# Performance work log

Hardware: AMD Instinct MI355X
Metric: run time of the kernel (lower is better)

The kernel has to match this reference:

```python
import jax, jax.numpy as jnp
import numpy as np

N, H, L, O = 8192, 512, 3, 512
LN_EPS = 1e-5


def setup_inputs() -> dict:
    key = jax.random.key(0)
    ks = jax.random.split(key, 8)
    # sparse symmetric adjacency with positive weights, zero diagonal
    u = jax.random.uniform(ks[0], (N, N))
    w = jax.random.uniform(ks[1], (N, N)) * 0.9 + 0.1
    A = jnp.where(u < 0.004, w, 0.0)
    A = (A + A.T) * 0.5
    A = A * (1.0 - jnp.eye(N, dtype=A.dtype))
    s = 0.02
    return {
        "node_feat": jax.random.normal(ks[2], (1, N, H), jnp.float32),
        "adj": A[None],
        "conv_w": jax.random.normal(ks[3], (L, H, H), jnp.float32) * s,
        "conv_b": jnp.zeros((L, H), jnp.float32),
        "mlp_w": jax.random.normal(ks[4], (L, H, H), jnp.float32) * s,
        "mlp_b": jnp.zeros((L, H), jnp.float32),
        "ln_g": jnp.ones((L, H), jnp.float32),
        "ln_b": jnp.zeros((L, H), jnp.float32),
        "lin_w": jax.random.normal(ks[5], (H, O), jnp.float32) * s,
        "lin_b": jnp.zeros((O,), jnp.float32),
    }


def _layer_norm(x, g, b):
    mu = jnp.mean(x, axis=-1, keepdims=True)
    var = jnp.mean(jnp.square(x - mu), axis=-1, keepdims=True)
    return (x - mu) * jax.lax.rsqrt(var + LN_EPS) * g + b


def reference(node_feat, adj, conv_w, conv_b, mlp_w, mlp_b, ln_g, ln_b, lin_w, lin_b):
    x = node_feat[0]          # [N, H]
    A = adj[0]                # [N, N]
    A = jnp.where(A > 0, A, 0.0)  # edges are positive entries only
    # gcn_norm: add self-loops (weight 1) only where missing
    d = jnp.diagonal(A)
    A1 = A + jnp.diag(jnp.where(d > 0, 0.0, 1.0))
    # deg scattered at target (edge_index[1] = column)
    deg = jnp.sum(A1, axis=0)
    dinv = jnp.where(deg > 0, deg ** -0.5, 0.0)
    Ahat = dinv[:, None] * A1 * dinv[None, :]  # [N, N]
    for l in range(L):
        # GCNConv: linear, propagate (aggregate at col), bias
        x = Ahat.T @ (x @ conv_w[l]) + conv_b[l]
        # MLP: Linear -> LayerNorm -> ReLU
        x = jax.nn.relu(_layer_norm(x @ mlp_w[l] + mlp_b[l], ln_g[l], ln_b[l]))
    mu = (x @ lin_w + lin_b)[None]  # [1, N, O]
    return mu
```

## Files before the change

### kernel.cpp

```cpp
#include <hip/hip_runtime.h>

#define NN 8192
#define HD 512
#define NL 3
#define CAP 128
#define NWB (273 * NL)
#define LN_EPS 1e-5f

typedef _Float16 f16;
typedef _Float16 f16x8 __attribute__((ext_vector_type(8)));
typedef _Float16 f16x4 __attribute__((ext_vector_type(4)));
typedef _Float16 f16x2 __attribute__((ext_vector_type(2)));
typedef float f32x4 __attribute__((ext_vector_type(4)));

__device__ __forceinline__ unsigned short f16_bits(f16 h) {
  union { f16 h; unsigned short u; } x; x.h = h; return x.u;
}
__device__ __forceinline__ f16 bits_f16(unsigned short u) {
  union { unsigned short u; f16 h; } x; x.u = u; return x.h;
}

__global__ __launch_bounds__(256) void k_prep(const float* __restrict__ A,
                                              const float* __restrict__ x0,
                                              const float* __restrict__ convw,
                                              const float* __restrict__ mlpw,
                                              const float* __restrict__ convb,
                                              const float* __restrict__ mlpb,
                                              const float* __restrict__ lw,
                                              unsigned* __restrict__ ell,
                                              int* __restrict__ nnz8,
                                              float* __restrict__ dinv,
                                              f16* __restrict__ xs,
                                              f16* __restrict__ WlT,
                                              float* __restrict__ bl,
                                              f16* __restrict__ lwT) {
  const int b = blockIdx.x;
  const int t = threadIdx.x;

  if (b < NWB) {
    const int l = b / 273;
    const int bx = b % 273;
    if (bx < 256) {
      const int m0 = bx * 2;
      const float* Wc = convw + (size_t)l * HD * HD;
      const float* Wm = mlpw + (size_t)l * HD * HD;
      f16* o = WlT + (size_t)l * HD * HD;
      float a00 = 0.f, a01 = 0.f, a10 = 0.f, a11 = 0.f;
      const float* wc0 = Wc + (size_t)m0 * HD;
      const float* wc1 = Wc + (size_t)(m0 + 1) * HD;
      for (int k = 0; k < HD; k++) {
        const float w0 = Wm[(size_t)k * HD + t];
        const float w1 = Wm[(size_t)k * HD + t + 256];
        const float c0 = wc0[k];
        const float c1 = wc1[k];
        a00 = fmaf(c0, w0, a00);
        a01 = fmaf(c0, w1, a01);
        a10 = fmaf(c1, w0, a10);
        a11 = fmaf(c1, w1, a11);
      }
      o[(size_t)t * HD + m0] = (f16)a00;
      o[(size_t)(t + 256) * HD + m0] = (f16)a01;
      o[(size_t)t * HD + m0 + 1] = (f16)a10;
      o[(size_t)(t + 256) * HD + m0 + 1] = (f16)a11;
    } else if (bx == 256) {
      const float* Wm = mlpw + (size_t)l * HD * HD;
      float acc0 = mlpb[l * HD + t];
      float acc1 = mlpb[l * HD + t + 256];
      for (int k = 0; k < HD; k++) {
        const float cb = convb[l * HD + k];
        acc0 = fmaf(cb, Wm[(size_t)k * HD + t], acc0);
        acc1 = fmaf(cb, Wm[(size_t)k * HD + t + 256], acc1);
      }
      bl[l * HD + t] = acc0;
      bl[l * HD + t + 256] = acc1;
    } else if (l == 0) {
      const int base = (bx - 257) * 16384;
      #pragma unroll 4
      for (int j = 0; j < 64; j++) {
        const int idx = base + j * 256 + t;
        const int k = idx >> 9, n = idx & 511;
        lwT[(size_t)n * HD + k] = (f16)lw[idx];
      }
    }
    return;
  }

  __shared__ int wtot[4];
  __shared__ float wsum[4];
  __shared__ float sdinv;
  const int r = b - NWB;
  const int lane = t & 63;
  const int wv = t >> 6;
  const float4* ar = (const float4*)(A + (size_t)r * NN);
  unsigned* er = ell + (size_t)r * CAP;
  const int rot = (r * 5) & 2047;

  int c = 0;
  float s = 0.f;
  #pragma unroll
  for (int i = 0; i < 8; i++) {
    const int f = (t + i * 256 + rot) & 2047;
    const float4 v = ar[f];
    c += (v.x > 0.f) + (v.y > 0.f) + (v.z > 0.f) + (v.w > 0.f);
    s += v.x + v.y + v.z + v.w;
  }
  int inc = c;
  #pragma unroll
  for (int d = 1; d < 64; d <<= 1) {
    int vv = __shfl_up(inc, d);
    if (lane >= d) inc += vv;
  }
  float ss = s;
  #pragma unroll
  for (int m = 1; m < 64; m <<= 1) ss += __shfl_xor(ss, m);
  if (lane == 63) wtot[wv] = inc;
  if (lane == 0) wsum[wv] = ss;
  __syncthreads();
  int base = inc - c;
  for (int w = 0; w < wv; w++) base += wtot[w];

  int o = base;
  #pragma unroll
  for (int i = 0; i < 8; i++) {
    const int f = (t + i * 256 + rot) & 2047;
    const float4 v = ar[f];
    float vals[4] = {v.x, v.y, v.z, v.w};
    #pragma unroll
    for (int q = 0; q < 4; q++) {
      float val = vals[q];
      if (val > 0.f) {
        if (o < CAP) er[o] = ((unsigned)f16_bits((f16)val) << 16) | (unsigned)(f * 4 + q);
        o++;
      }
    }
  }
  if (t == 255) {
    int ne = wtot[0] + wtot[1] + wtot[2] + wtot[3];
    if (ne < CAP) er[ne] = (0x3C00u << 16) | (unsigned)r;
    int ne1 = ne + 1; if (ne1 > CAP) ne1 = CAP;
    int n8 = (ne1 + 7) & ~7;
    for (int k = ne1; k < n8; k++) er[k] = (unsigned)r;
    nnz8[r] = n8;
    float deg = wsum[0] + wsum[1] + wsum[2] + wsum[3] + 1.f;
    float di = rsqrtf(deg);
    dinv[r] = di;
    sdinv = di;
  }
  __syncthreads();
  {
    const float di = sdinv;
    const float2 xv = ((const float2*)(x0 + (size_t)r * HD))[t];
    f16x2 o2 = {(f16)(xv.x * di), (f16)(xv.y * di)};
    ((f16x2*)(xs + (size_t)r * HD))[t] = o2;
  }
}

__global__ __launch_bounds__(256) void k_spmm(const unsigned* __restrict__ ell,
                                              const int* __restrict__ nnz8,
                                              const float* __restrict__ dinv,
                                              const f16* __restrict__ xs,
                                              f16* __restrict__ y) {
  const int bid = blockIdx.x;
  const int chunk = bid & 3;
  const int rb = bid >> 2;
  const int r = __builtin_amdgcn_readfirstlane(rb * 4 + (threadIdx.x >> 6));
  const int lane = threadIdx.x & 63;
  const int c0 = chunk * 128 + lane * 2;
  const uint4* er = (const uint4*)(ell + (size_t)r * CAP);
  const int ne = nnz8[r];
  const f16* xc = xs + c0;
  float a0 = 0.f, a1 = 0.f;
  for (int e8 = 0; e8 < (ne >> 3); e8++) {
    const uint4 ea = er[e8 * 2];
    const uint4 eb = er[e8 * 2 + 1];
    unsigned wv[8] = {ea.x, ea.y, ea.z, ea.w, eb.x, eb.y, eb.z, eb.w};
    f16x2 xv[8];
    #pragma unroll
    for (int q = 0; q < 8; q++)
      xv[q] = *(const f16x2*)(xc + (size_t)(wv[q] & 0xFFFFu) * HD);
    #pragma unroll
    for (int q = 0; q < 8; q++) {
      const float fw = (float)bits_f16((unsigned short)(wv[q] >> 16));
      a0 = fmaf(fw, (float)xv[q][0], a0);
      a1 = fmaf(fw, (float)xv[q][1], a1);
    }
  }
  const float s = dinv[r];
  f16x2 o = {(f16)(a0 * s), (f16)(a1 * s)};
  *(f16x2*)(y + (size_t)r * HD + c0) = o;
}

__global__ __launch_bounds__(512) void k_gemm_ln(const f16* __restrict__ y,
                                                 const f16* __restrict__ WT,
                                                 const float* __restrict__ bias,
                                                 const float* __restrict__ g,
                                                 const float* __restrict__ bb,
                                                 const float* __restrict__ dscale,
                                                 f16* __restrict__ outp) {
  __shared__ float red[32][4][2];
  const int t = threadIdx.x;
  const int lane = t & 63;
  const int w = t >> 6;
  const int wm = w >> 2;
  const int wn = w & 3;
  const int m0 = blockIdx.x * 32;
  const int rl = lane & 15, kg = (lane >> 4) * 8;
  const f16* aP = y + (size_t)(m0 + wm * 16 + rl) * HD + kg;
  const f16* bP = WT + (size_t)(wn * 128 + rl) * HD + kg;

  f32x4 acc[8];
  #pragma unroll
  for (int j = 0; j < 8; j++) { f32x4 z = {0.f, 0.f, 0.f, 0.f}; acc[j] = z; }

  #pragma unroll 2
  for (int ks = 0; ks < HD; ks += 32) {
    const f16x8 af = *(const f16x8*)(aP + ks);
    #pragma unroll
    for (int j = 0; j < 8; j++) {
      const f16x8 bf = *(const f16x8*)(bP + (size_t)j * 16 * HD + ks);
      acc[j] = __builtin_amdgcn_mfma_f32_16x16x32_f16(af, bf, acc[j], 0, 0, 0);
    }
  }

  const int cg = lane >> 4, cl = lane & 15;
  float av[8][4];
  #pragma unroll
  for (int j = 0; j < 8; j++) {
    const float bv = bias[wn * 128 + j * 16 + cl];
    #pragma unroll
    for (int r = 0; r < 4; r++) av[j][r] = acc[j][r] + bv;
  }
  #pragma unroll
  for (int r = 0; r < 4; r++) {
    float s = 0.f, sq = 0.f;
    #pragma unroll
    for (int j = 0; j < 8; j++) { s += av[j][r]; sq += av[j][r] * av[j][r]; }
    #pragma unroll
    for (int m = 1; m < 16; m <<= 1) { s += __shfl_xor(s, m); sq += __shfl_xor(sq, m); }
    if (cl == 0) {
      red[wm * 16 + cg * 4 + r][wn][0] = s;
      red[wm * 16 + cg * 4 + r][wn][1] = sq;
    }
  }
  __syncthreads();
  #pragma unroll
  for (int r = 0; r < 4; r++) {
    const int rb = wm * 16 + cg * 4 + r;
    float s = 0.f, sq = 0.f;
    #pragma unroll
    for (int q = 0; q < 4; q++) { s += red[rb][q][0]; sq += red[rb][q][1]; }
    const float mu = s * (1.f / HD);
    const float rs = rsqrtf(sq * (1.f / HD) - mu * mu + LN_EPS);
    const int row = m0 + rb;
    const float dsc = dscale ? dscale[row] : 1.f;
    #pragma unroll
    for (int j = 0; j < 8; j++) {
      const int col = wn * 128 + j * 16 + cl;
      const float val = fmaxf((av[j][r] - mu) * rs * g[col] + bb[col], 0.f) * dsc;
      outp[(size_t)row * HD + col] = (f16)val;
    }
  }
}

__global__ __launch_bounds__(256) void k_gemm_direct(const f16* __restrict__ A,
                                                     const f16* __restrict__ BT,
                                                     float* __restrict__ C,
                                                     const float* __restrict__ bias) {
  const int t = threadIdx.x;
  const int lane = t & 63;
  const int wave = t >> 6;
  const int wm = wave >> 1, wn = wave & 1;
  const int m0 = blockIdx.x * 128, n0 = blockIdx.y * 128;
  const int rl = lane & 15, kg = (lane >> 4) * 8;

  const f16* aP[4];
  const f16* bP[4];
  #pragma unroll
  for (int i = 0; i < 4; i++)
    aP[i] = A + (size_t)(m0 + wm * 64 + i * 16 + rl) * HD + kg;
  #pragma unroll
  for (int j = 0; j < 4; j++)
    bP[j] = BT + (size_t)(n0 + wn * 64 + j * 16 + rl) * HD + kg;

  f32x4 acc[4][4];
  #pragma unroll
  for (int i = 0; i < 4; i++)
    #pragma unroll
    for (int j = 0; j < 4; j++) {
      f32x4 z = {0.f, 0.f, 0.f, 0.f};
      acc[i][j] = z;
    }

  #pragma unroll 4
  for (int ks = 0; ks < HD; ks += 32) {
    f16x8 af[4], bf[4];
    #pragma unroll
    for (int i = 0; i < 4; i++) af[i] = *(const f16x8*)(aP[i] + ks);
    #pragma unroll
    for (int j = 0; j < 4; j++) bf[j] = *(const f16x8*)(bP[j] + ks);
    #pragma unroll
    for (int i = 0; i < 4; i++)
      #pragma unroll
      for (int j = 0; j < 4; j++)
        acc[i][j] = __builtin_amdgcn_mfma_f32_16x16x32_f16(af[i], bf[j], acc[i][j], 0, 0, 0);
  }

  const int cg = lane >> 4, cl = lane & 15;
  #pragma unroll
  for (int i = 0; i < 4; i++) {
    #pragma unroll
    for (int j = 0; j < 4; j++) {
      const int col = n0 + wn * 64 + j * 16 + cl;
      const float bv = bias ? bias[col] : 0.f;
      #pragma unroll
      for (int rr = 0; rr < 4; rr++) {
        const int row = m0 + wm * 64 + i * 16 + cg * 4 + rr;
        C[(size_t)row * HD + col] = acc[i][j][rr] + bv;
      }
    }
  }
}

extern "C" void kernel_launch(void* const* d_in, const int* in_sizes, int n_in,
                              void* d_out, int out_size, void* d_ws, size_t ws_size,
                              hipStream_t stream) {
  const float* node_feat = (const float*)d_in[0];
  const float* adj       = (const float*)d_in[1];
  const float* conv_w    = (const float*)d_in[2];
  const float* conv_b    = (const float*)d_in[3];
  const float* mlp_w     = (const float*)d_in[4];
  const float* mlp_b     = (const float*)d_in[5];
  const float* ln_g      = (const float*)d_in[6];
  const float* ln_b      = (const float*)d_in[7];
  const float* lin_w     = (const float*)d_in[8];
  const float* lin_b     = (const float*)d_in[9];
  float* out = (float*)d_out;

  char* p = (char*)d_ws;
  unsigned* ell = (unsigned*)p; p += (size_t)NN * CAP * 4;
  int* nnz8  = (int*)p;   p += (size_t)NN * 4;
  float* dinv = (float*)p; p += (size_t)NN * 4;
  f16* xsA   = (f16*)p;   p += (size_t)NN * HD * 2;
  f16* xsB   = (f16*)p;   p += (size_t)NN * HD * 2;
  f16* ybuf  = (f16*)p;   p += (size_t)NN * HD * 2;
  f16* WlT   = (f16*)p;   p += (size_t)NL * HD * HD * 2;
  f16* lwT   = (f16*)p;   p += (size_t)HD * HD * 2;
  float* bl  = (float*)p; p += (size_t)NL * HD * 4;

  k_prep<<<NWB + NN, 256, 0, stream>>>(adj, node_feat, conv_w, mlp_w,
                                       conv_b, mlp_b, lin_w,
                                       ell, nnz8, dinv, xsA, WlT, bl, lwT);

  f16* xcur = xsA;
  for (int l = 0; l < NL; l++) {
    k_spmm<<<NN, 256, 0, stream>>>(ell, nnz8, dinv, xcur, ybuf);
    f16* nxt = (xcur == xsA) ? xsB : xsA;
    k_gemm_ln<<<NN / 32, 512, 0, stream>>>(ybuf, WlT + (size_t)l * HD * HD,
                                           bl + l * HD, ln_g + l * HD, ln_b + l * HD,
                                           (l < 2) ? dinv : nullptr, nxt);
    xcur = nxt;
  }
  k_gemm_direct<<<dim3(64, 4), 256, 0, stream>>>(xcur, lwT, out, lin_b);
}
```

Baseline: 332.5 us.

## Split adjacency row scan into four segment blocks with separate degree kernel

The prep kernel now scans each adjacency row with four blocks, one per 2048-column segment, instead of one block per row. Each segment writes its own ELL slice of capacity 48 and stores a partial degree sum. A new small kernel combines the partial sums into dinv and scales the input features. The aim is more memory-level parallelism on the dominant 256 MB adjacency read. In exchange it adds a kernel launch, per-segment padding that the SpMM must loop over, and a per-segment overflow cap that could drop edges in a dense segment.

```diff
diff --git a/kernel.cpp b/kernel.cpp
--- a/kernel.cpp
+++ b/kernel.cpp
@@ -3,7 +3,8 @@
 #define NN 8192
 #define HD 512
 #define NL 3
-#define CAP 128
+#define CAPQ 48
+#define CAPR (4 * CAPQ)
 #define NWB (273 * NL)
 #define LN_EPS 1e-5f
 
@@ -21,16 +22,14 @@
 }
 
 __global__ __launch_bounds__(256) void k_prep(const float* __restrict__ A,
-                                              const float* __restrict__ x0,
                                               const float* __restrict__ convw,
                                               const float* __restrict__ mlpw,
                                               const float* __restrict__ convb,
                                               const float* __restrict__ mlpb,
                                               const float* __restrict__ lw,
                                               unsigned* __restrict__ ell,
-                                              int* __restrict__ nnz8,
-                                              float* __restrict__ dinv,
-                                              f16* __restrict__ xs,
+                                              int* __restrict__ nnz8q,
+                                              float* __restrict__ psum,
                                               f16* __restrict__ WlT,
                                               float* __restrict__ bl,
                                               f16* __restrict__ lwT) {
@@ -87,23 +86,20 @@
 
   __shared__ int wtot[4];
   __shared__ float wsum[4];
-  __shared__ float sdinv;
-  const int r = b - NWB;
+  const int sb = b - NWB;
+  const int r = sb >> 2;
+  const int seg = sb & 3;
   const int lane = t & 63;
   const int wv = t >> 6;
-  const float4* ar = (const float4*)(A + (size_t)r * NN);
-  unsigned* er = ell + (size_t)r * CAP;
-  const int rot = (r * 5) & 2047;
-
-  int c = 0;
-  float s = 0.f;
-  #pragma unroll
-  for (int i = 0; i < 8; i++) {
-    const int f = (t + i * 256 + rot) & 2047;
-    const float4 v = ar[f];
-    c += (v.x > 0.f) + (v.y > 0.f) + (v.z > 0.f) + (v.w > 0.f);
-    s += v.x + v.y + v.z + v.w;
-  }
+  const float4* aseg = (const float4*)(A + (size_t)r * NN + seg * 2048);
+  unsigned* er = ell + (size_t)r * CAPR + seg * CAPQ;
+
+  const float4 v0 = aseg[t];
+  const float4 v1 = aseg[t + 256];
+  int c = (v0.x > 0.f) + (v0.y > 0.f) + (v0.z > 0.f) + (v0.w > 0.f) +
+          (v1.x > 0.f) + (v1.y > 0.f) + (v1.z > 0.f) + (v1.w > 0.f);
+  float s = v0.x + v0.y + v0.z + v0.w + v1.x + v1.y + v1.z + v1.w;
+
   int inc = c;
   #pragma unroll
   for (int d = 1; d < 64; d <<= 1) {
@@ -120,43 +116,59 @@
   for (int w = 0; w < wv; w++) base += wtot[w];
 
   int o = base;
-  #pragma unroll
-  for (int i = 0; i < 8; i++) {
-    const int f = (t + i * 256 + rot) & 2047;
-    const float4 v = ar[f];
-    float vals[4] = {v.x, v.y, v.z, v.w};
+  const int cb0 = seg * 2048 + t * 4;
+  const int cb1 = seg * 2048 + (t + 256) * 4;
+  {
+    float vals[4] = {v0.x, v0.y, v0.z, v0.w};
     #pragma unroll
     for (int q = 0; q < 4; q++) {
-      float val = vals[q];
-      if (val > 0.f) {
-        if (o < CAP) er[o] = ((unsigned)f16_bits((f16)val) << 16) | (unsigned)(f * 4 + q);
+      if (vals[q] > 0.f) {
+        if (o < CAPQ) er[o] = ((unsigned)f16_bits((f16)vals[q]) << 16) | (unsigned)(cb0 + q);
+        o++;
+      }
+    }
+  }
+  {
+    float vals[4] = {v1.x, v1.y, v1.z, v1.w};
+    #pragma unroll
+    for (int q = 0; q < 4; q++) {
+      if (vals[q] > 0.f) {
+        if (o < CAPQ) er[o] = ((unsigned)f16_bits((f16)vals[q]) << 16) | (unsigned)(cb1 + q);
         o++;
       }
     }
   }
   if (t == 255) {
     int ne = wtot[0] + wtot[1] + wtot[2] + wtot[3];
-    if (ne < CAP) er[ne] = (0x3C00u << 16) | (unsigned)r;
-    int ne1 = ne + 1; if (ne1 > CAP) ne1 = CAP;
-    int n8 = (ne1 + 7) & ~7;
-    for (int k = ne1; k < n8; k++) er[k] = (unsigned)r;
-    nnz8[r] = n8;
-    float deg = wsum[0] + wsum[1] + wsum[2] + wsum[3] + 1.f;
-    float di = rsqrtf(deg);
-    dinv[r] = di;
-    sdinv = di;
-  }
-  __syncthreads();
-  {
-    const float di = sdinv;
-    const float2 xv = ((const float2*)(x0 + (size_t)r * HD))[t];
-    f16x2 o2 = {(f16)(xv.x * di), (f16)(xv.y * di)};
-    ((f16x2*)(xs + (size_t)r * HD))[t] = o2;
-  }
+    if (ne > CAPQ) ne = CAPQ;
+    const bool own = (seg == (r >> 11));
+    if (own && ne < CAPQ) { er[ne] = (0x3C00u << 16) | (unsigned)r; ne++; }
+    const int n8 = (ne + 7) & ~7;
+    for (int k = ne; k < n8; k++) er[k] = (unsigned)r;
+    nnz8q[r * 4 + seg] = n8;
+    psum[r * 4 + seg] = wsum[0] + wsum[1] + wsum[2] + wsum[3];
+  }
+}
+
+__global__ __launch_bounds__(256) void k_deg(const float* __restrict__ psum,
+                                             const float* __restrict__ x0,
+                                             float* __restrict__ dinv,
+                                             f16* __restrict__ xs) {
+  const int r = blockIdx.x * 4 + (threadIdx.x >> 6);
+  const int lane = threadIdx.x & 63;
+  const float4 ps = *(const float4*)(psum + (size_t)r * 4);
+  const float di = rsqrtf(ps.x + ps.y + ps.z + ps.w + 1.f);
+  if (lane == 0) dinv[r] = di;
+  const float4* xr = (const float4*)(x0 + (size_t)r * HD);
+  const float4 a = xr[lane * 2];
+  const float4 bq = xr[lane * 2 + 1];
+  f16x8 o = {(f16)(a.x * di), (f16)(a.y * di), (f16)(a.z * di), (f16)(a.w * di),
+             (f16)(bq.x * di), (f16)(bq.y * di), (f16)(bq.z * di), (f16)(bq.w * di)};
+  *(f16x8*)(xs + (size_t)r * HD + lane * 8) = o;
 }
 
 __global__ __launch_bounds__(256) void k_spmm(const unsigned* __restrict__ ell,
-                                              const int* __restrict__ nnz8,
+                                              const int* __restrict__ nnz8q,
                                               const float* __restrict__ dinv,
                                               const f16* __restrict__ xs,
                                               f16* __restrict__ y) {
@@ -166,23 +178,29 @@
   const int r = __builtin_amdgcn_readfirstlane(rb * 4 + (threadIdx.x >> 6));
   const int lane = threadIdx.x & 63;
   const int c0 = chunk * 128 + lane * 2;
-  const uint4* er = (const uint4*)(ell + (size_t)r * CAP);
-  const int ne = nnz8[r];
+  const unsigned* erow = ell + (size_t)r * CAPR;
+  const int4 nn = *(const int4*)(nnz8q + (size_t)r * 4);
+  const int ne8s[4] = {nn.x >> 3, nn.y >> 3, nn.z >> 3, nn.w >> 3};
   const f16* xc = xs + c0;
   float a0 = 0.f, a1 = 0.f;
-  for (int e8 = 0; e8 < (ne >> 3); e8++) {
-    const uint4 ea = er[e8 * 2];
-    const uint4 eb = er[e8 * 2 + 1];
-    unsigned wv[8] = {ea.x, ea.y, ea.z, ea.w, eb.x, eb.y, eb.z, eb.w};
-    f16x2 xv[8];
-    #pragma unroll
-    for (int q = 0; q < 8; q++)
-      xv[q] = *(const f16x2*)(xc + (size_t)(wv[q] & 0xFFFFu) * HD);
-    #pragma unroll
-    for (int q = 0; q < 8; q++) {
-      const float fw = (float)bits_f16((unsigned short)(wv[q] >> 16));
-      a0 = fmaf(fw, (float)xv[q][0], a0);
-      a1 = fmaf(fw, (float)xv[q][1], a1);
+  #pragma unroll
+  for (int seg = 0; seg < 4; seg++) {
+    const uint4* er = (const uint4*)(erow + seg * CAPQ);
+    const int ne8 = ne8s[seg];
+    for (int e8 = 0; e8 < ne8; e8++) {
+      const uint4 ea = er[e8 * 2];
+      const uint4 eb = er[e8 * 2 + 1];
+      unsigned wv[8] = {ea.x, ea.y, ea.z, ea.w, eb.x, eb.y, eb.z, eb.w};
+      f16x2 xv[8];
+      #pragma unroll
+      for (int q = 0; q < 8; q++)
+        xv[q] = *(const f16x2*)(xc + (size_t)(wv[q] & 0xFFFFu) * HD);
+      #pragma unroll
+      for (int q = 0; q < 8; q++) {
+        const float fw = (float)bits_f16((unsigned short)(wv[q] >> 16));
+        a0 = fmaf(fw, (float)xv[q][0], a0);
+        a1 = fmaf(fw, (float)xv[q][1], a1);
+      }
     }
   }
   const float s = dinv[r];
@@ -337,8 +355,9 @@
   float* out = (float*)d_out;
 
   char* p = (char*)d_ws;
-  unsigned* ell = (unsigned*)p; p += (size_t)NN * CAP * 4;
-  int* nnz8  = (int*)p;   p += (size_t)NN * 4;
+  unsigned* ell = (unsigned*)p; p += (size_t)NN * CAPR * 4;
+  int* nnz8q = (int*)p;  p += (size_t)NN * 4 * 4;
+  float* psum = (float*)p; p += (size_t)NN * 4 * 4;
   float* dinv = (float*)p; p += (size_t)NN * 4;
   f16* xsA   = (f16*)p;   p += (size_t)NN * HD * 2;
   f16* xsB   = (f16*)p;   p += (size_t)NN * HD * 2;
@@ -347,13 +366,13 @@
   f16* lwT   = (f16*)p;   p += (size_t)HD * HD * 2;
   float* bl  = (float*)p; p += (size_t)NL * HD * 4;
 
-  k_prep<<<NWB + NN, 256, 0, stream>>>(adj, node_feat, conv_w, mlp_w,
-                                       conv_b, mlp_b, lin_w,
-                                       ell, nnz8, dinv, xsA, WlT, bl, lwT);
+  k_prep<<<NWB + 4 * NN, 256, 0, stream>>>(adj, conv_w, mlp_w, conv_b, mlp_b,
+                                           lin_w, ell, nnz8q, psum, WlT, bl, lwT);
+  k_deg<<<NN / 4, 256, 0, stream>>>(psum, node_feat, dinv, xsA);
 
   f16* xcur = xsA;
   for (int l = 0; l < NL; l++) {
-    k_spmm<<<NN, 256, 0, stream>>>(ell, nnz8, dinv, xcur, ybuf);
+    k_spmm<<<NN, 256, 0, stream>>>(ell, nnz8q, dinv, xcur, ybuf);
     f16* nxt = (xcur == xsA) ? xsB : xsA;
     k_gemm_ln<<<NN / 32, 512, 0, stream>>>(ybuf, WlT + (size_t)l * HD * HD,
                                            bl + l * HD, ln_g + l * HD, ln_b + l * HD,
```

After: 329.3 us. Within noise of the previous version (-1.0%).
